# Optimization experiments

Measured on AMD Instinct MI355X. Metric: run time of the kernel, lower is better.

The kernel has to match this reference:

```python
import jax, jax.numpy as jnp
import numpy as np

M = 64          # SOM grid rows
N_GRID = 64     # SOM grid cols
DIM = 768       # SapBERT hidden size
COMPS = M * N_GRID
NBATCH = 8192   # number of embedded vectors per step


def setup_inputs() -> dict:
    key = jax.random.key(0)
    k1, k2 = jax.random.split(key)
    embedded = jax.random.normal(k1, (NBATCH, DIM), dtype=jnp.float32)
    contents = jax.random.normal(k2, (M, N_GRID, DIM), dtype=jnp.float32)
    # grid_dists: squared pairwise distances between grid coordinates (pdist2 in init_grid)
    x, y = np.meshgrid(range(M), range(N_GRID))
    g = np.stack([x, y]).reshape(2, -1).astype(np.float32)  # [2, comps]
    sq = (g ** 2).sum(0)
    gd = sq[:, None] + sq[None, :] - 2.0 * (g.T @ g)
    grid_dists = jnp.asarray(gd, dtype=jnp.float32)
    sigma = jnp.float32(max(M, N_GRID) / 2.0)
    return {"embedded": embedded, "contents": contents,
            "grid_dists": grid_dists, "sigma": sigma}


def reference(embedded, contents, grid_dists, sigma):
    comps = grid_dists.shape[0]
    dim = embedded.shape[1]
    flat_c = contents.reshape(comps, dim)
    # Gaussian neighborhood weights (compute_weight, weighted=True)
    weights = jnp.exp(-grid_dists / (2.0 * sigma ** 2))  # [comps, comps]
    # find_bmu: squared L2 dist + argmin (expanded form, same argmin as
    # the materialized N x comps x dim diff tensor in the original)
    dist = ((embedded ** 2).sum(-1, keepdims=True)
            + (flat_c ** 2).sum(-1)[None, :]
            - 2.0 * embedded @ flat_c.T)                 # [N, comps]
    min_idx = jnp.argmin(dist, axis=1)                   # [N]
    # scatter-accumulate counts and sums per codebook entry (index_add_)
    freq = jnp.zeros((comps,), embedded.dtype).at[min_idx].add(1.0)
    sums = jnp.zeros((comps, dim), embedded.dtype).at[min_idx].add(embedded)
    used = freq > 0
    avg = jnp.where(used[:, None], sums / jnp.maximum(freq, 1.0)[:, None], flat_c)
    # freq_weights[i,j] = weights[i,j] * freq[i]; update_num = sum_j fw[i,j]*avg[j,d]
    num = freq[:, None] * (weights @ avg)                # [comps, dim]
    denom = freq * weights.sum(axis=1)                   # [comps]
    update = num / jnp.where(used, denom, 1.0)[:, None]
    new_flat = jnp.where(used[:, None], update, flat_c)  # only update_denom!=0 rows
    new_contents = new_flat.reshape(contents.shape)
    delta = jnp.linalg.norm(new_contents - contents, axis=-1).sum()
    return delta, new_contents
```

## Files before the change

kernel.cpp:

```cpp
#include <hip/hip_runtime.h>

#define NB 8192
#define COMPS 4096
#define DIM 768

typedef _Float16 half8_t __attribute__((ext_vector_type(8)));
typedef float floatx4 __attribute__((ext_vector_type(4)));
typedef unsigned short ushort4_t __attribute__((ext_vector_type(4)));
typedef unsigned long long ullx2 __attribute__((ext_vector_type(2)));

typedef __attribute__((address_space(1))) const void* gas_ptr;
typedef __attribute__((address_space(3))) void* las_ptr;

__device__ __forceinline__ void gl_lds16(const _Float16* g, _Float16* l) {
  __builtin_amdgcn_global_load_lds((gas_ptr)(const void*)g, (las_ptr)(void*)l, 16, 0, 0);
}

__device__ __forceinline__ unsigned long long pack_min(float v, int col) {
  unsigned u = __float_as_uint(v);
  u = (u & 0x80000000u) ? ~u : (u | 0x80000000u);
  return ((unsigned long long)u << 32) | (unsigned)col;
}

#define PREP_GRID 13401
__global__ void k_prep(const float* __restrict__ e, const float* __restrict__ c,
                       const float* __restrict__ sigma,
                       _Float16* __restrict__ ehi,
                       _Float16* __restrict__ chi, _Float16* __restrict__ clo,
                       float* __restrict__ cnorm, float* __restrict__ E,
                       float* __restrict__ rE, float* __restrict__ sums,
                       float* __restrict__ freq, float* __restrict__ rowsq,
                       unsigned long long* __restrict__ packed,
                       unsigned int* __restrict__ done) {
  int bx = blockIdx.x, t = threadIdx.x;
  if (bx < 6144) {
    int id = bx * 256 + t;
    float4 v = ((const float4*)e)[id];
    ushort4_t h;
    float xs[4] = {v.x, v.y, v.z, v.w};
#pragma unroll
    for (int q = 0; q < 4; ++q)
      h[q] = __builtin_bit_cast(unsigned short, (_Float16)xs[q]);
    ((ushort4_t*)ehi)[id] = h;
  } else if (bx < 10240) {
    int i = bx - 6144;
    float s = 0.f;
    if (t < 192) {
      float4 v = ((const float4*)c)[i * 192 + t];
      float xs[4] = {v.x, v.y, v.z, v.w};
      ushort4_t h, l;
#pragma unroll
      for (int q = 0; q < 4; ++q) {
        _Float16 hh = (_Float16)xs[q];
        _Float16 ll = (_Float16)(xs[q] - (float)hh);
        h[q] = __builtin_bit_cast(unsigned short, hh);
        l[q] = __builtin_bit_cast(unsigned short, ll);
        s = fmaf(xs[q], xs[q], s);
      }
      ((ushort4_t*)chi)[i * 192 + t] = h;
      ((ushort4_t*)clo)[i * 192 + t] = l;
    }
#pragma unroll
    for (int o = 32; o; o >>= 1) s += __shfl_down(s, o);
    __shared__ float red[3];
    if (t < 192 && (t & 63) == 0) red[t >> 6] = s;
    __syncthreads();
    if (t == 0) cnorm[i] = red[0] + red[1] + red[2];
  } else if (bx < 10304) {
    int i = bx - 10240;
    if (t < 64) {
      float sg = sigma[0];
      float inv = -1.0f / (2.0f * sg * sg);
      float d = (float)(i - t);
      float v = expf(d * d * inv);
      E[i * 64 + t] = v;
      float s = v;
#pragma unroll
      for (int o = 32; o; o >>= 1) s += __shfl_down(s, o);
      if (t == 0) rE[i] = s;
    }
  } else if (bx < 13376) {
    int id = (bx - 10304) * 256 + t;
    floatx4 z = {0.f, 0.f, 0.f, 0.f};
    ((floatx4*)sums)[id] = z;
  } else if (bx < 13392) {
    int id = (bx - 13376) * 256 + t;
    ullx2 f = {~0ULL, ~0ULL};
    ((ullx2*)packed)[id] = f;
  } else if (bx < 13396) {
    int id = (bx - 13392) * 256 + t;
    floatx4 z = {0.f, 0.f, 0.f, 0.f};
    ((floatx4*)freq)[id] = z;
  } else if (bx < 13400) {
    int id = (bx - 13396) * 256 + t;
    floatx4 z = {0.f, 0.f, 0.f, 0.f};
    ((floatx4*)rowsq)[id] = z;
  } else {
    if (t == 0) *done = 0u;
  }
}

__launch_bounds__(256)
__global__ void k_gemm1(const _Float16* __restrict__ ehi,
                        const _Float16* __restrict__ chi, const _Float16* __restrict__ clo,
                        const float* __restrict__ cnorm,
                        unsigned long long* __restrict__ packed) {
  __shared__ _Float16 lds[3][128 * 64];
  int tid = threadIdx.x;
  int lane = tid & 63, w = tid >> 6;
  int wr = w >> 1, wc = w & 1;
  int g = lane >> 4, rl = lane & 15;
  int i0 = blockIdx.x * 128, j0 = blockIdx.y * 128;

  int lr = lane >> 3, lc = lane & 7;
  int cch = lc ^ lr;
  const _Float16* gsrc = ehi;
  _Float16* dst = &lds[0][0];
  if (w == 0)      { gsrc = ehi + (size_t)i0 * DIM; dst = &lds[0][0]; }
  else if (w == 1) { gsrc = chi + (size_t)j0 * DIM; dst = &lds[1][0]; }
  else if (w == 2) { gsrc = clo + (size_t)j0 * DIM; dst = &lds[2][0]; }
  gsrc += (size_t)lr * DIM + cch * 8;
  dst += lane * 8;

  floatx4 acc[4][4] = {};

  for (int kt = 0; kt < DIM; kt += 64) {
    __syncthreads();
    if (w < 3) {
#pragma unroll
      for (int q = 0; q < 16; ++q)
        gl_lds16(gsrc + kt + (size_t)(q * 8) * DIM, dst + q * 512);
    }
    __syncthreads();

#pragma unroll
    for (int s = 0; s < 2; ++s) {
      half8_t ah[4];
#pragma unroll
      for (int m = 0; m < 4; ++m) {
        int r = wr * 64 + m * 16 + rl;
        int p = (s * 4 + g) ^ (rl & 7);
        ah[m] = *(half8_t*)&lds[0][r * 64 + p * 8];
      }
#pragma unroll
      for (int n = 0; n < 4; ++n) {
        int r = wc * 64 + n * 16 + rl;
        int p = (s * 4 + g) ^ (rl & 7);
        half8_t bh = *(half8_t*)&lds[1][r * 64 + p * 8];
        half8_t bl = *(half8_t*)&lds[2][r * 64 + p * 8];
#pragma unroll
        for (int m = 0; m < 4; ++m) {
          acc[m][n] = __builtin_amdgcn_mfma_f32_16x16x32_f16(ah[m], bh, acc[m][n], 0, 0, 0);
          acc[m][n] = __builtin_amdgcn_mfma_f32_16x16x32_f16(ah[m], bl, acc[m][n], 0, 0, 0);
        }
      }
    }
  }

  float cn[4];
#pragma unroll
  for (int n = 0; n < 4; ++n) cn[n] = cnorm[j0 + wc * 64 + n * 16 + rl];

#pragma unroll
  for (int m = 0; m < 4; ++m) {
#pragma unroll
    for (int j = 0; j < 4; ++j) {
      int row = i0 + wr * 64 + m * 16 + g * 4 + j;
      float best = 3.0e38f;
      int bcol = 0;
#pragma unroll
      for (int n = 0; n < 4; ++n) {
        float d = fmaf(-2.0f, acc[m][n][j], cn[n]);
        int col = j0 + wc * 64 + n * 16 + rl;
        if (d < best) { best = d; bcol = col; }
      }
      unsigned long long pk = pack_min(best, bcol);
#pragma unroll
      for (int o = 1; o < 16; o <<= 1) {
        unsigned long long other = __shfl_xor(pk, o);
        if (other < pk) pk = other;
      }
      if (rl == 0) atomicMin(&packed[row], pk);
    }
  }
}

__global__ void k_scatter(const float* __restrict__ e,
                          const unsigned long long* __restrict__ packed,
                          float* __restrict__ freq, float* __restrict__ sums) {
  int i = blockIdx.x, t = threadIdx.x;
  int idx = (int)(packed[i] & 0xffffffffULL);
  if (t == 0) unsafeAtomicAdd(&freq[idx], 1.0f);
#pragma unroll
  for (int r = 0; r < 3; ++r) {
    int d = t + 256 * r;
    unsafeAtomicAdd(&sums[(size_t)idx * DIM + d], e[(size_t)i * DIM + d]);
  }
}

__global__ void k_t1(const float* __restrict__ sums, const float* __restrict__ freq,
                     const float* __restrict__ cont, const float* __restrict__ E,
                     float* __restrict__ T1) {
  __shared__ float S[64 * 128];
  __shared__ float Esh[64 * 64];
  int a = blockIdx.x, db = blockIdx.y, t = threadIdx.x;
#pragma unroll
  for (int it = 0; it < 8; ++it) {
    int id = t + 256 * it;
    int row = id >> 5, c4 = id & 31;
    int comp = a * 64 + row;
    float f = freq[comp];
    size_t o = (size_t)comp * 192 + db * 32 + c4;
    floatx4 v;
    if (f > 0.f) {
      floatx4 sv = ((const floatx4*)sums)[o];
      v = sv * (1.0f / f);
    } else v = ((const floatx4*)cont)[o];
    ((floatx4*)S)[id] = v;
  }
#pragma unroll
  for (int it = 0; it < 4; ++it) {
    int id = t + 256 * it;
    ((floatx4*)Esh)[id] = ((const floatx4*)E)[id];
  }
  __syncthreads();

  int d4 = t & 31, b0 = (t >> 5) * 8;
  floatx4 acc[8] = {};
  for (int bp = 0; bp < 64; ++bp) {
    floatx4 sv = ((floatx4*)S)[bp * 32 + d4];
#pragma unroll
    for (int b = 0; b < 8; ++b)
      acc[b] += Esh[(b0 + b) * 64 + bp] * sv;
  }
#pragma unroll
  for (int b = 0; b < 8; ++b)
    ((floatx4*)T1)[(size_t)(a * 64 + b0 + b) * 192 + db * 32 + d4] = acc[b];
}

__global__ void k_wnum(const float* __restrict__ T1, const float* __restrict__ E,
                       const float* __restrict__ rE, const float* __restrict__ freq,
                       const float* __restrict__ cont, float* __restrict__ out,
                       float* __restrict__ rowsq, unsigned int* __restrict__ done) {
  __shared__ float S[64 * 128];
  __shared__ float Esh[64 * 64];
  int b = blockIdx.x, db = blockIdx.y, t = threadIdx.x;
#pragma unroll
  for (int it = 0; it < 8; ++it) {
    int id = t + 256 * it;
    int ap = id >> 5, c4 = id & 31;
    ((floatx4*)S)[id] = ((const floatx4*)T1)[(size_t)(ap * 64 + b) * 192 + db * 32 + c4];
  }
#pragma unroll
  for (int it = 0; it < 4; ++it) {
    int id = t + 256 * it;
    ((floatx4*)Esh)[id] = ((const floatx4*)E)[id];
  }
  __syncthreads();

  int d4 = t & 31, a0 = (t >> 5) * 8;
  floatx4 acc[8] = {};
  for (int ap = 0; ap < 64; ++ap) {
    floatx4 tv = ((floatx4*)S)[ap * 32 + d4];
#pragma unroll
    for (int a = 0; a < 8; ++a)
      acc[a] += Esh[(a0 + a) * 64 + ap] * tv;
  }

  float rb = rE[b];
  float sq[8];
#pragma unroll
  for (int a = 0; a < 8; ++a) {
    int comp = (a0 + a) * 64 + b;
    bool used = freq[comp] > 0.f;
    floatx4 cv = ((const floatx4*)cont)[(size_t)comp * 192 + db * 32 + d4];
    floatx4 val;
    if (used) val = acc[a] * (1.0f / (rE[a0 + a] * rb));
    else val = cv;
    size_t base = 1 + (size_t)comp * DIM + db * 128 + d4 * 4;
    out[base] = val[0]; out[base + 1] = val[1];
    out[base + 2] = val[2]; out[base + 3] = val[3];
    floatx4 df = val - cv;
    sq[a] = df[0] * df[0] + df[1] * df[1] + df[2] * df[2] + df[3] * df[3];
  }
#pragma unroll
  for (int a = 0; a < 8; ++a) {
#pragma unroll
    for (int o = 1; o < 32; o <<= 1) sq[a] += __shfl_xor(sq[a], o);
  }
  if (d4 == 0) {
#pragma unroll
    for (int a = 0; a < 8; ++a)
      unsafeAtomicAdd(&rowsq[(a0 + a) * 64 + b], sq[a]);
  }

  __shared__ unsigned int lastflag;
  __syncthreads();
  if (t == 0) {
    __threadfence();
    unsigned int old = atomicAdd(done, 1u);
    lastflag = (old == 64u * 6u - 1u) ? 1u : 0u;
  }
  __syncthreads();
  if (lastflag) {
    double s = 0.0;
    for (int c2 = t; c2 < COMPS; c2 += 256) {
      float r = __hip_atomic_load(&rowsq[c2], __ATOMIC_RELAXED,
                                  __HIP_MEMORY_SCOPE_AGENT);
      s += sqrt((double)r);
    }
#pragma unroll
    for (int o = 32; o; o >>= 1) s += __shfl_down(s, o);
    __shared__ double red[4];
    if ((t & 63) == 0) red[t >> 6] = s;
    __syncthreads();
    if (t == 0) out[0] = (float)(red[0] + red[1] + red[2] + red[3]);
  }
}

extern "C" void kernel_launch(void* const* d_in, const int* in_sizes, int n_in,
                              void* d_out, int out_size, void* d_ws, size_t ws_size,
                              hipStream_t stream) {
  const float* e = (const float*)d_in[0];
  const float* cont = (const float*)d_in[1];
  const float* sigma = (const float*)d_in[3];
  float* out = (float*)d_out;

  char* ws = (char*)d_ws;
  size_t off = 0;
  auto take = [&](size_t bytes) { char* p = ws + off; off += (bytes + 255) & ~(size_t)255; return p; };

  unsigned long long* packed = (unsigned long long*)take(NB * 8);
  float* freq  = (float*)take(COMPS * 4);
  float* rowsq = (float*)take(COMPS * 4);
  float* cnorm = (float*)take(COMPS * 4);
  float* E     = (float*)take(64 * 64 * 4);
  float* rE    = (float*)take(64 * 4);
  unsigned int* done = (unsigned int*)take(256);
  float* sums  = (float*)take((size_t)COMPS * DIM * 4);
  char* U = take((size_t)NB * DIM * 2 + (size_t)COMPS * DIM * 2 * 2);
  _Float16* ehi = (_Float16*)U;
  _Float16* chi = (_Float16*)(U + (size_t)NB * DIM * 2);
  _Float16* clo = (_Float16*)(U + (size_t)NB * DIM * 2 + (size_t)COMPS * DIM * 2);
  float* T1 = (float*)(U + (size_t)NB * DIM * 2);

  k_prep<<<PREP_GRID, 256, 0, stream>>>(e, cont, sigma, ehi, chi, clo,
                                        cnorm, E, rE, sums, freq, rowsq,
                                        packed, done);
  k_gemm1<<<dim3(NB / 128, COMPS / 128), 256, 0, stream>>>(ehi, chi, clo, cnorm, packed);
  k_scatter<<<NB, 256, 0, stream>>>(e, packed, freq, sums);
  k_t1<<<dim3(64, 6), 256, 0, stream>>>(sums, freq, cont, E, T1);
  k_wnum<<<dim3(64, 6), 256, 0, stream>>>(T1, E, rE, freq, cont, out, rowsq, done);
}
```

Measured before the change: 307.0 us.

## Fuse scatter and separable neighborhood GEMMs into one persistent grid-barrier kernel

Replaces the atomic float scatter of 8192x768 values into a zeroed sums buffer with a counting sort: per-component counts, a prefix scan, and a row index list. Each component's mean is then gathered directly from the embedded rows. The scatter, T1 and wnum stages are merged into a single 384-block kernel that uses software grid barriers. This drops the 12MB sums zeroing, the float atomics and two launch gaps. In exchange it relies on all 384 blocks being co-resident for the spin barriers, runs the scan on a single block, and does the gather serially per component.

```diff
diff --git a/kernel.cpp b/kernel.cpp
--- a/kernel.cpp
+++ b/kernel.cpp
@@ -3,11 +3,13 @@
 #define NB 8192
 #define COMPS 4096
 #define DIM 768
+#define TB 384
 
 typedef _Float16 half8_t __attribute__((ext_vector_type(8)));
 typedef float floatx4 __attribute__((ext_vector_type(4)));
 typedef unsigned short ushort4_t __attribute__((ext_vector_type(4)));
 typedef unsigned long long ullx2 __attribute__((ext_vector_type(2)));
+typedef int intx4 __attribute__((ext_vector_type(4)));
 
 typedef __attribute__((address_space(1))) const void* gas_ptr;
 typedef __attribute__((address_space(3))) void* las_ptr;
@@ -22,16 +24,16 @@
   return ((unsigned long long)u << 32) | (unsigned)col;
 }
 
-#define PREP_GRID 13401
+#define PREP_GRID 10329
 __global__ void k_prep(const float* __restrict__ e, const float* __restrict__ c,
                        const float* __restrict__ sigma,
                        _Float16* __restrict__ ehi,
                        _Float16* __restrict__ chi, _Float16* __restrict__ clo,
                        float* __restrict__ cnorm, float* __restrict__ E,
-                       float* __restrict__ rE, float* __restrict__ sums,
-                       float* __restrict__ freq, float* __restrict__ rowsq,
+                       float* __restrict__ rE, int* __restrict__ cnt,
+                       float* __restrict__ rowsq,
                        unsigned long long* __restrict__ packed,
-                       unsigned int* __restrict__ done) {
+                       unsigned int* __restrict__ tk) {
   int bx = blockIdx.x, t = threadIdx.x;
   if (bx < 6144) {
     int id = bx * 256 + t;
@@ -79,24 +81,20 @@
       for (int o = 32; o; o >>= 1) s += __shfl_down(s, o);
       if (t == 0) rE[i] = s;
     }
-  } else if (bx < 13376) {
+  } else if (bx < 10320) {
     int id = (bx - 10304) * 256 + t;
-    floatx4 z = {0.f, 0.f, 0.f, 0.f};
-    ((floatx4*)sums)[id] = z;
-  } else if (bx < 13392) {
-    int id = (bx - 13376) * 256 + t;
     ullx2 f = {~0ULL, ~0ULL};
     ((ullx2*)packed)[id] = f;
-  } else if (bx < 13396) {
-    int id = (bx - 13392) * 256 + t;
-    floatx4 z = {0.f, 0.f, 0.f, 0.f};
-    ((floatx4*)freq)[id] = z;
-  } else if (bx < 13400) {
-    int id = (bx - 13396) * 256 + t;
+  } else if (bx < 10324) {
+    int id = (bx - 10320) * 256 + t;
+    intx4 z = {0, 0, 0, 0};
+    ((intx4*)cnt)[id] = z;
+  } else if (bx < 10328) {
+    int id = (bx - 10324) * 256 + t;
     floatx4 z = {0.f, 0.f, 0.f, 0.f};
     ((floatx4*)rowsq)[id] = z;
   } else {
-    if (t == 0) *done = 0u;
+    if (t < 64) tk[t] = 0u;
   }
 }
 
@@ -185,136 +183,198 @@
   }
 }
 
-__global__ void k_scatter(const float* __restrict__ e,
-                          const unsigned long long* __restrict__ packed,
-                          float* __restrict__ freq, float* __restrict__ sums) {
-  int i = blockIdx.x, t = threadIdx.x;
-  int idx = (int)(packed[i] & 0xffffffffULL);
-  if (t == 0) unsafeAtomicAdd(&freq[idx], 1.0f);
-#pragma unroll
-  for (int r = 0; r < 3; ++r) {
-    int d = t + 256 * r;
-    unsafeAtomicAdd(&sums[(size_t)idx * DIM + d], e[(size_t)i * DIM + d]);
-  }
-}
-
-__global__ void k_t1(const float* __restrict__ sums, const float* __restrict__ freq,
-                     const float* __restrict__ cont, const float* __restrict__ E,
-                     float* __restrict__ T1) {
+__device__ __forceinline__ void gbar(unsigned int* tkslot) {
+  __syncthreads();
+  if (threadIdx.x == 0) {
+    __hip_atomic_fetch_add(tkslot, 1u, __ATOMIC_RELEASE, __HIP_MEMORY_SCOPE_AGENT);
+    while (__hip_atomic_load(tkslot, __ATOMIC_ACQUIRE, __HIP_MEMORY_SCOPE_AGENT)
+           < (unsigned)TB) {
+      __builtin_amdgcn_s_sleep(8);
+    }
+  }
+  __syncthreads();
+}
+
+__launch_bounds__(256, 2)
+__global__ void k_tail(const float* __restrict__ e,
+                       const unsigned long long* __restrict__ packed,
+                       const float* __restrict__ cont, const float* __restrict__ E,
+                       const float* __restrict__ rE, int* __restrict__ cnt,
+                       int* __restrict__ offs, int* __restrict__ cursor,
+                       int* __restrict__ rows, float* __restrict__ T1,
+                       float* __restrict__ rowsq, float* __restrict__ out,
+                       unsigned int* __restrict__ tk) {
   __shared__ float S[64 * 128];
   __shared__ float Esh[64 * 64];
-  int a = blockIdx.x, db = blockIdx.y, t = threadIdx.x;
-#pragma unroll
-  for (int it = 0; it < 8; ++it) {
-    int id = t + 256 * it;
-    int row = id >> 5, c4 = id & 31;
-    int comp = a * 64 + row;
-    float f = freq[comp];
-    size_t o = (size_t)comp * 192 + db * 32 + c4;
-    floatx4 v;
-    if (f > 0.f) {
-      floatx4 sv = ((const floatx4*)sums)[o];
-      v = sv * (1.0f / f);
-    } else v = ((const floatx4*)cont)[o];
-    ((floatx4*)S)[id] = v;
+  int bid = blockIdx.x, t = threadIdx.x;
+  int gtid = bid * 256 + t;
+
+  if (gtid < NB) {
+    int idx = (int)(packed[gtid] & 0xffffffffULL);
+    atomicAdd(&cnt[idx], 1);
   }
 #pragma unroll
   for (int it = 0; it < 4; ++it) {
     int id = t + 256 * it;
     ((floatx4*)Esh)[id] = ((const floatx4*)E)[id];
   }
-  __syncthreads();
-
-  int d4 = t & 31, b0 = (t >> 5) * 8;
-  floatx4 acc[8] = {};
-  for (int bp = 0; bp < 64; ++bp) {
-    floatx4 sv = ((floatx4*)S)[bp * 32 + d4];
-#pragma unroll
-    for (int b = 0; b < 8; ++b)
-      acc[b] += Esh[(b0 + b) * 64 + bp] * sv;
-  }
-#pragma unroll
-  for (int b = 0; b < 8; ++b)
-    ((floatx4*)T1)[(size_t)(a * 64 + b0 + b) * 192 + db * 32 + d4] = acc[b];
-}
-
-__global__ void k_wnum(const float* __restrict__ T1, const float* __restrict__ E,
-                       const float* __restrict__ rE, const float* __restrict__ freq,
-                       const float* __restrict__ cont, float* __restrict__ out,
-                       float* __restrict__ rowsq, unsigned int* __restrict__ done) {
-  __shared__ float S[64 * 128];
-  __shared__ float Esh[64 * 64];
-  int b = blockIdx.x, db = blockIdx.y, t = threadIdx.x;
-#pragma unroll
-  for (int it = 0; it < 8; ++it) {
-    int id = t + 256 * it;
-    int ap = id >> 5, c4 = id & 31;
-    ((floatx4*)S)[id] = ((const floatx4*)T1)[(size_t)(ap * 64 + b) * 192 + db * 32 + c4];
-  }
-#pragma unroll
-  for (int it = 0; it < 4; ++it) {
-    int id = t + 256 * it;
-    ((floatx4*)Esh)[id] = ((const floatx4*)E)[id];
-  }
-  __syncthreads();
-
-  int d4 = t & 31, a0 = (t >> 5) * 8;
-  floatx4 acc[8] = {};
-  for (int ap = 0; ap < 64; ++ap) {
-    floatx4 tv = ((floatx4*)S)[ap * 32 + d4];
-#pragma unroll
-    for (int a = 0; a < 8; ++a)
-      acc[a] += Esh[(a0 + a) * 64 + ap] * tv;
-  }
-
-  float rb = rE[b];
-  float sq[8];
-#pragma unroll
-  for (int a = 0; a < 8; ++a) {
-    int comp = (a0 + a) * 64 + b;
-    bool used = freq[comp] > 0.f;
-    floatx4 cv = ((const floatx4*)cont)[(size_t)comp * 192 + db * 32 + d4];
-    floatx4 val;
-    if (used) val = acc[a] * (1.0f / (rE[a0 + a] * rb));
-    else val = cv;
-    size_t base = 1 + (size_t)comp * DIM + db * 128 + d4 * 4;
-    out[base] = val[0]; out[base + 1] = val[1];
-    out[base + 2] = val[2]; out[base + 3] = val[3];
-    floatx4 df = val - cv;
-    sq[a] = df[0] * df[0] + df[1] * df[1] + df[2] * df[2] + df[3] * df[3];
-  }
-#pragma unroll
-  for (int a = 0; a < 8; ++a) {
-#pragma unroll
-    for (int o = 1; o < 32; o <<= 1) sq[a] += __shfl_xor(sq[a], o);
-  }
-  if (d4 == 0) {
-#pragma unroll
-    for (int a = 0; a < 8; ++a)
-      unsafeAtomicAdd(&rowsq[(a0 + a) * 64 + b], sq[a]);
-  }
-
-  __shared__ unsigned int lastflag;
-  __syncthreads();
-  if (t == 0) {
-    __threadfence();
-    unsigned int old = atomicAdd(done, 1u);
-    lastflag = (old == 64u * 6u - 1u) ? 1u : 0u;
-  }
-  __syncthreads();
-  if (lastflag) {
-    double s = 0.0;
-    for (int c2 = t; c2 < COMPS; c2 += 256) {
-      float r = __hip_atomic_load(&rowsq[c2], __ATOMIC_RELAXED,
-                                  __HIP_MEMORY_SCOPE_AGENT);
-      s += sqrt((double)r);
-    }
-#pragma unroll
-    for (int o = 32; o; o >>= 1) s += __shfl_down(s, o);
-    __shared__ double red[4];
-    if ((t & 63) == 0) red[t >> 6] = s;
-    __syncthreads();
-    if (t == 0) out[0] = (float)(red[0] + red[1] + red[2] + red[3]);
+  gbar(&tk[0]);
+
+  if (bid == 0) {
+    int v[16];
+    int tot = 0;
+#pragma unroll
+    for (int q = 0; q < 16; ++q) { v[q] = cnt[t * 16 + q]; tot += v[q]; }
+    int lane = t & 63, wid = t >> 6;
+    int s = tot;
+#pragma unroll
+    for (int o = 1; o < 64; o <<= 1) {
+      int u = __shfl_up(s, o);
+      if (lane >= o) s += u;
+    }
+    __shared__ int wt[4];
+    if (lane == 63) wt[wid] = s;
+    __syncthreads();
+    int add = 0;
+    for (int w2 = 0; w2 < wid; ++w2) add += wt[w2];
+    int run = add + s - tot;
+#pragma unroll
+    for (int q = 0; q < 16; ++q) {
+      __hip_atomic_store(&offs[t * 16 + q], run, __ATOMIC_RELAXED,
+                         __HIP_MEMORY_SCOPE_AGENT);
+      __hip_atomic_store(&cursor[t * 16 + q], run, __ATOMIC_RELAXED,
+                         __HIP_MEMORY_SCOPE_AGENT);
+      run += v[q];
+    }
+  }
+  gbar(&tk[1]);
+
+  if (gtid < NB) {
+    int idx = (int)(packed[gtid] & 0xffffffffULL);
+    int pos = atomicAdd(&cursor[idx], 1);
+    __hip_atomic_store(&rows[pos], gtid, __ATOMIC_RELAXED,
+                       __HIP_MEMORY_SCOPE_AGENT);
+  }
+  gbar(&tk[2]);
+
+  {
+    int a = bid / 6, db = bid % 6;
+    int wv = t >> 6, lane = t & 63;
+    const float2* e2 = (const float2*)e;
+    const float2* c2 = (const float2*)cont;
+#pragma unroll 1
+    for (int rr = 0; rr < 16; ++rr) {
+      int r = wv * 16 + rr;
+      int comp = a * 64 + r;
+      int n = cnt[comp];
+      float2 acc2 = {0.f, 0.f};
+      if (n == 0) {
+        acc2 = c2[(size_t)comp * 384 + db * 64 + lane];
+      } else {
+        int o0 = __hip_atomic_load(&offs[comp], __ATOMIC_RELAXED,
+                                   __HIP_MEMORY_SCOPE_AGENT);
+        for (int k = 0; k < n; ++k) {
+          int i = __hip_atomic_load(&rows[o0 + k], __ATOMIC_RELAXED,
+                                    __HIP_MEMORY_SCOPE_AGENT);
+          float2 ev = e2[(size_t)i * 384 + db * 64 + lane];
+          acc2.x += ev.x; acc2.y += ev.y;
+        }
+        float inv = 1.0f / (float)n;
+        acc2.x *= inv; acc2.y *= inv;
+      }
+      S[r * 128 + lane * 2] = acc2.x;
+      S[r * 128 + lane * 2 + 1] = acc2.y;
+    }
+    __syncthreads();
+
+    int d4 = t & 31, b0 = (t >> 5) * 8;
+    floatx4 acc[8] = {};
+    for (int bp = 0; bp < 64; ++bp) {
+      floatx4 sv = ((floatx4*)S)[bp * 32 + d4];
+#pragma unroll
+      for (int b = 0; b < 8; ++b)
+        acc[b] += Esh[(b0 + b) * 64 + bp] * sv;
+    }
+#pragma unroll
+    for (int b = 0; b < 8; ++b) {
+      size_t base = ((size_t)(a * 64 + b0 + b) * 192 + db * 32 + d4) * 4;
+#pragma unroll
+      for (int q = 0; q < 4; ++q)
+        __hip_atomic_store(&T1[base + q], acc[b][q], __ATOMIC_RELAXED,
+                           __HIP_MEMORY_SCOPE_AGENT);
+    }
+  }
+  gbar(&tk[3]);
+
+  {
+    int b = bid / 6, db = bid % 6;
+#pragma unroll
+    for (int it = 0; it < 8; ++it) {
+      int id = t + 256 * it;
+      int ap = id >> 5, c4 = id & 31;
+      ((floatx4*)S)[id] =
+          ((const floatx4*)T1)[(size_t)(ap * 64 + b) * 192 + db * 32 + c4];
+    }
+    __syncthreads();
+
+    int d4 = t & 31, a0 = (t >> 5) * 8;
+    floatx4 acc[8] = {};
+    for (int ap = 0; ap < 64; ++ap) {
+      floatx4 tv = ((floatx4*)S)[ap * 32 + d4];
+#pragma unroll
+      for (int a = 0; a < 8; ++a)
+        acc[a] += Esh[(a0 + a) * 64 + ap] * tv;
+    }
+
+    float rb = rE[b];
+    float sq[8];
+#pragma unroll
+    for (int a = 0; a < 8; ++a) {
+      int comp = (a0 + a) * 64 + b;
+      bool used = cnt[comp] > 0;
+      floatx4 cv = ((const floatx4*)cont)[(size_t)comp * 192 + db * 32 + d4];
+      floatx4 val;
+      if (used) val = acc[a] * (1.0f / (rE[a0 + a] * rb));
+      else val = cv;
+      size_t base = 1 + (size_t)comp * DIM + db * 128 + d4 * 4;
+      out[base] = val[0]; out[base + 1] = val[1];
+      out[base + 2] = val[2]; out[base + 3] = val[3];
+      floatx4 df = val - cv;
+      sq[a] = df[0] * df[0] + df[1] * df[1] + df[2] * df[2] + df[3] * df[3];
+    }
+#pragma unroll
+    for (int a = 0; a < 8; ++a) {
+#pragma unroll
+      for (int o = 1; o < 32; o <<= 1) sq[a] += __shfl_xor(sq[a], o);
+    }
+    if (d4 == 0) {
+#pragma unroll
+      for (int a = 0; a < 8; ++a)
+        unsafeAtomicAdd(&rowsq[(a0 + a) * 64 + b], sq[a]);
+    }
+
+    __shared__ unsigned int lastflag;
+    __syncthreads();
+    if (t == 0) {
+      unsigned int old = __hip_atomic_fetch_add(&tk[4], 1u, __ATOMIC_ACQ_REL,
+                                                __HIP_MEMORY_SCOPE_AGENT);
+      lastflag = (old == (unsigned)TB - 1u) ? 1u : 0u;
+    }
+    __syncthreads();
+    if (lastflag) {
+      double s = 0.0;
+      for (int c2i = t; c2i < COMPS; c2i += 256) {
+        float r = __hip_atomic_load(&rowsq[c2i], __ATOMIC_RELAXED,
+                                    __HIP_MEMORY_SCOPE_AGENT);
+        s += sqrt((double)r);
+      }
+#pragma unroll
+      for (int o = 32; o; o >>= 1) s += __shfl_down(s, o);
+      __shared__ double red[4];
+      if ((t & 63) == 0) red[t >> 6] = s;
+      __syncthreads();
+      if (t == 0) out[0] = (float)(red[0] + red[1] + red[2] + red[3]);
+    }
   }
 }
 
@@ -331,13 +391,15 @@
   auto take = [&](size_t bytes) { char* p = ws + off; off += (bytes + 255) & ~(size_t)255; return p; };
 
   unsigned long long* packed = (unsigned long long*)take(NB * 8);
-  float* freq  = (float*)take(COMPS * 4);
+  int* cnt    = (int*)take(COMPS * 4);
+  int* offs   = (int*)take(COMPS * 4);
+  int* cursor = (int*)take(COMPS * 4);
+  int* rows   = (int*)take(NB * 4);
   float* rowsq = (float*)take(COMPS * 4);
   float* cnorm = (float*)take(COMPS * 4);
   float* E     = (float*)take(64 * 64 * 4);
   float* rE    = (float*)take(64 * 4);
-  unsigned int* done = (unsigned int*)take(256);
-  float* sums  = (float*)take((size_t)COMPS * DIM * 4);
+  unsigned int* tk = (unsigned int*)take(256);
   char* U = take((size_t)NB * DIM * 2 + (size_t)COMPS * DIM * 2 * 2);
   _Float16* ehi = (_Float16*)U;
   _Float16* chi = (_Float16*)(U + (size_t)NB * DIM * 2);
@@ -345,10 +407,8 @@
   float* T1 = (float*)(U + (size_t)NB * DIM * 2);
 
   k_prep<<<PREP_GRID, 256, 0, stream>>>(e, cont, sigma, ehi, chi, clo,
-                                        cnorm, E, rE, sums, freq, rowsq,
-                                        packed, done);
+                                        cnorm, E, rE, cnt, rowsq, packed, tk);
   k_gemm1<<<dim3(NB / 128, COMPS / 128), 256, 0, stream>>>(ehi, chi, clo, cnorm, packed);
-  k_scatter<<<NB, 256, 0, stream>>>(e, packed, freq, sums);
-  k_t1<<<dim3(64, 6), 256, 0, stream>>>(sums, freq, cont, E, T1);
-  k_wnum<<<dim3(64, 6), 256, 0, stream>>>(T1, E, rE, freq, cont, out, rowsq, done);
-}
+  k_tail<<<TB, 256, 0, stream>>>(e, packed, cont, E, rE, cnt, offs, cursor,
+                                 rows, T1, rowsq, out, tk);
+}
```

New measurement: 1.220 ms. +297.4%, slower.
